# Optimization experiments

Hardware: AMD Instinct MI355X
Metric: run time of the kernel (lower is better)

The kernel has to match this reference:

```python
import jax, jax.numpy as jnp
import numpy as np

EPS = 1e-12


def _phi(e):
    # e: [C, L] -> pairwise euclidean distances [C, C], diagonal zeroed
    sq = jnp.sum(e * e, axis=1)                      # [C]
    prod = e @ e.T                                   # [C, C]
    d2 = sq[:, None] + sq[None, :] - 2.0 * prod
    d = jnp.sqrt(jnp.clip(d2, EPS, None))
    C = e.shape[0]
    return d * (1.0 - jnp.eye(C, dtype=e.dtype))


def setup_inputs() -> dict:
    key = jax.random.key(0)
    k1, k2, k3 = jax.random.split(key, 3)
    N, C, L = 64, 512, 256
    le_student = jax.random.normal(k1, (N, C, L), dtype=jnp.float32)
    le_teacher = jax.random.normal(k2, (N, C, L), dtype=jnp.float32)
    targets = jax.random.randint(k3, (N, C), 0, 2, dtype=jnp.int32)
    return {"le_student": le_student, "le_teacher": le_teacher, "targets": targets}


def reference(le_student, le_teacher, targets):
    N, C, L = le_student.shape
    m = targets.astype(le_student.dtype)             # [N, C] 0/1 mask
    es = le_student * m[:, :, None]                  # zero out negative rows
    et = le_teacher * m[:, :, None]

    Ds = jax.vmap(_phi)(es)                          # [N, C, C]
    Dt = jax.vmap(_phi)(et)                          # [N, C, C]

    eye = jnp.eye(C, dtype=m.dtype)
    pm = m[:, :, None] * m[:, None, :]               # pairs of positive rows
    offdiag = pm * (1.0 - eye)                       # off-diagonal positive pairs

    npos = jnp.sum(m, axis=1)                        # [N]
    cnt = npos * (npos - 1.0)                        # entries with d > 0 in submatrix
    valid = npos > 1.0
    safe_cnt = jnp.maximum(cnt, 1.0)

    mean_s = jnp.sum(Ds * offdiag, axis=(1, 2)) / safe_cnt
    mean_t = jax.lax.stop_gradient(jnp.sum(Dt * offdiag, axis=(1, 2)) / safe_cnt)
    mean_s = jnp.where(valid, mean_s, 1.0)
    mean_t = jnp.where(valid, mean_t, 1.0)

    d = Ds / mean_s[:, None, None]
    td = jax.lax.stop_gradient(Dt / mean_t[:, None, None])

    diff = d - td
    adiff = jnp.abs(diff)
    huber = jnp.where(adiff < 1.0, 0.5 * diff * diff, adiff - 0.5)

    per = jnp.sum(huber * pm, axis=(1, 2)) / jnp.maximum(npos, 1.0)
    return jnp.sum(jnp.where(valid, per, 0.0))
```

## Files before the change

### kernel.cpp

```cpp
#include <hip/hip_runtime.h>
#include <hip/hip_bf16.h>
#include <hip/hip_fp16.h>
#include <math.h>

#define NB 64
#define CC 512
#define LL 256

typedef __attribute__((ext_vector_type(4))) float floatx4;
typedef __attribute__((ext_vector_type(8))) short short8;

static __device__ __forceinline__ unsigned f2bf2(float x, float y) {
    __hip_bfloat162 h = __float22bfloat162_rn(make_float2(x, y));
    union { __hip_bfloat162 h; unsigned u; } c; c.h = h;
    return c.u;
}
static __device__ __forceinline__ unsigned f2h(float x) {
    __half h = __float2half_rn(x);
    union { __half h; unsigned short u; } c; c.h = h;
    return (unsigned)c.u;
}
static __device__ __forceinline__ float h2f(unsigned u) {
    union { unsigned short u; __half h; } c; c.u = (unsigned short)u;
    return __half2float(c.h);
}

__global__ __launch_bounds__(256) void prep_kernel(
    const int* __restrict__ targets,
    int* __restrict__ idx, int* __restrict__ npos,
    float* __restrict__ sumS, float* __restrict__ sumT, float* __restrict__ out)
{
    const int n = blockIdx.x, tid = threadIdx.x;
    __shared__ int s_cnt[8], s_off[8];
    const int w = tid >> 6, lane = tid & 63;
    const int* tg = targets + n * CC;
    const bool p0 = tg[tid] != 0;
    const bool p1 = tg[tid + 256] != 0;
    const unsigned long long m0 = __ballot(p0);
    const unsigned long long m1 = __ballot(p1);
    if (lane == 0) { s_cnt[w] = __popcll(m0); s_cnt[4 + w] = __popcll(m1); }
    __syncthreads();
    if (tid == 0) {
        int a = 0;
        for (int i = 0; i < 8; ++i) { s_off[i] = a; a += s_cnt[i]; }
        npos[n] = a;
        sumS[n] = 0.0f; sumT[n] = 0.0f;
        if (n == 0) out[0] = 0.0f;
    }
    __syncthreads();
    const unsigned long long below = (1ull << lane) - 1ull;
    if (p0) idx[n * CC + s_off[w] + __popcll(m0 & below)] = tid;
    if (p1) idx[n * CC + s_off[4 + w] + __popcll(m1 & below)] = tid + 256;
}

static __device__ __forceinline__ bool decode_tile(int t, int u, int& tI, int& tJ) {
    if (t >= (u * (u + 1)) >> 1) return false;
    tI = 0;
    while (t >= u - tI) { t -= u - tI; ++tI; }
    tJ = tI + t;
    return true;
}

__global__ __launch_bounds__(256) void dist_kernel(
    const float* __restrict__ S, const float* __restrict__ T,
    const int* __restrict__ idx, const int* __restrict__ npos,
    float* __restrict__ sumS, float* __restrict__ sumT,
    unsigned* __restrict__ D)
{
    const int bx = blockIdx.x;
    const int n = bx / 36;
    const int np = npos[n];
    if (np < 2) return;
    int tI, tJ;
    if (!decode_tile(bx - n * 36, (np + 63) >> 6, tI, tJ)) return;
    const bool diag = (tI == tJ);

    __shared__ __align__(16) unsigned short lds[4][2][64][40];
    __shared__ float s_norm[4][64];
    __shared__ float redA[4], redB[4];

    const int tid = threadIdx.x;
    const int w = tid >> 6, lane = tid & 63;

    const bool stager = (!diag) || ((w & 1) == 0);
    const char* Pbase = (const char*)(((w >> 1) ? T : S) + (size_t)n * CC * LL);
    const int tileBase = ((w & 1) ? tJ : tI) * 64;
    const int r8 = lane >> 3, c8 = lane & 7;
    unsigned off_[8];
    #pragma unroll
    for (int i = 0; i < 8; ++i) {
        const int gk = tileBase + r8 + 8 * i;
        const int row = idx[n * CC + ((gk < np) ? gk : 0)];
        off_[i] = (unsigned)(row * LL * 4 + c8 * 16);
    }

    float4 pre[8];
    float nprt[8];
    #pragma unroll
    for (int i = 0; i < 8; ++i) nprt[i] = 0.0f;
    if (stager) {
        #pragma unroll
        for (int i = 0; i < 8; ++i) pre[i] = *(const float4*)(Pbase + off_[i]);
    }

    const int m16 = lane & 15, quad = lane >> 4;
    const int bufB = diag ? 0 : 1;
    const int wrow = w * 16;

    floatx4 accS[4], accT[4];
    #pragma unroll
    for (int c = 0; c < 4; ++c) {
        accS[c][0] = 0; accS[c][1] = 0; accS[c][2] = 0; accS[c][3] = 0;
        accT[c][0] = 0; accT[c][1] = 0; accT[c][2] = 0; accT[c][3] = 0;
    }

    for (int kk = 0; kk < 8; ++kk) {
        const int pb = kk & 1;
        if (stager) {
            #pragma unroll
            for (int i = 0; i < 8; ++i) {
                nprt[i] += pre[i].x * pre[i].x + pre[i].y * pre[i].y +
                           pre[i].z * pre[i].z + pre[i].w * pre[i].w;
                *(uint2*)&lds[w][pb][r8 + 8 * i][c8 * 4] =
                    make_uint2(f2bf2(pre[i].x, pre[i].y), f2bf2(pre[i].z, pre[i].w));
            }
        }
        __syncthreads();
        if (stager && kk < 7) {
            #pragma unroll
            for (int i = 0; i < 8; ++i)
                pre[i] = *(const float4*)(Pbase + off_[i] + (kk + 1) * 128);
        }
        const int aoff = (wrow + m16) * 40 + quad * 8;
        const short8 a_s = *(const short8*)(&lds[0][pb][0][0] + aoff);
        const short8 a_t = *(const short8*)(&lds[2][pb][0][0] + aoff);
        #pragma unroll
        for (int c = 0; c < 4; ++c) {
            const int boff = (c * 16 + m16) * 40 + quad * 8;
            const short8 b_s = *(const short8*)(&lds[bufB][pb][0][0] + boff);
            const short8 b_t = *(const short8*)(&lds[2 + bufB][pb][0][0] + boff);
            accS[c] = __builtin_amdgcn_mfma_f32_16x16x32_bf16(a_s, b_s, accS[c], 0, 0, 0);
            accT[c] = __builtin_amdgcn_mfma_f32_16x16x32_bf16(a_t, b_t, accT[c], 0, 0, 0);
        }
    }

    if (stager) {
        #pragma unroll
        for (int i = 0; i < 8; ++i) {
            float v = nprt[i];
            v += __shfl_xor(v, 1); v += __shfl_xor(v, 2); v += __shfl_xor(v, 4);
            if (c8 == 0) s_norm[w][r8 + 8 * i] = v;
        }
    }
    __syncthreads();

    unsigned* Dn = D + ((size_t)bx << 12);
    float l0 = 0.0f, l1 = 0.0f;
    #pragma unroll
    for (int c = 0; c < 4; ++c) {
        const int colL = c * 16 + m16;
        const int gj = tJ * 64 + colL;
        const float nBs = s_norm[bufB][colL];
        const float nBt = s_norm[2 + bufB][colL];
        #pragma unroll
        for (int r = 0; r < 4; ++r) {
            const int rowL = wrow + quad * 4 + r;
            const int gi = tI * 64 + rowL;
            const float ds = sqrtf(fmaxf(s_norm[0][rowL] + nBs - 2.0f * accS[c][r], 1e-12f));
            const float dt = sqrtf(fmaxf(s_norm[2][rowL] + nBt - 2.0f * accT[c][r], 1e-12f));
            if (gi < np && gj < np && gi != gj) { l0 += ds; l1 += dt; }
            Dn[rowL * 64 + colL] = f2h(ds) | (f2h(dt) << 16);
        }
    }

    #pragma unroll
    for (int o = 32; o; o >>= 1) { l0 += __shfl_down(l0, o); l1 += __shfl_down(l1, o); }
    if (lane == 0) { redA[w] = l0; redB[w] = l1; }
    __syncthreads();
    if (tid == 0) {
        const float wgt = diag ? 1.0f : 2.0f;
        atomicAdd(&sumS[n], wgt * (redA[0] + redA[1] + redA[2] + redA[3]));
        atomicAdd(&sumT[n], wgt * (redB[0] + redB[1] + redB[2] + redB[3]));
    }
}

__global__ __launch_bounds__(256) void huber_kernel(
    const unsigned* __restrict__ D, const int* __restrict__ npos,
    const float* __restrict__ sumS, const float* __restrict__ sumT,
    float* __restrict__ out)
{
    const int bx = blockIdx.x;
    const int n = bx / 36;
    const int np = npos[n];
    if (np < 2) return;
    int tI, tJ;
    if (!decode_tile(bx - n * 36, (np + 63) >> 6, tI, tJ)) return;

    const float cnt = (float)np * (float)(np - 1);
    const float inv_ms = cnt / sumS[n];
    const float inv_mt = cnt / sumT[n];

    const uint4* Dn = (const uint4*)(D + ((size_t)bx << 12));
    const int tid = threadIdx.x;

    float h = 0.0f;
    #pragma unroll
    for (int it = 0; it < 4; ++it) {
        const int e4 = it * 256 + tid;
        const uint4 v = Dn[e4];
        const unsigned vv[4] = { v.x, v.y, v.z, v.w };
        const int e0 = e4 * 4;
        #pragma unroll
        for (int k = 0; k < 4; ++k) {
            const int e = e0 + k;
            const int gi = tI * 64 + (e >> 6);
            const int gj = tJ * 64 + (e & 63);
            if (gi < np && gj < np && gi != gj) {
                const float ds = h2f(vv[k] & 0xffffu);
                const float dt = h2f(vv[k] >> 16);
                const float diff = ds * inv_ms - dt * inv_mt;
                const float ad = fabsf(diff);
                h += (ad < 1.0f) ? 0.5f * diff * diff : ad - 0.5f;
            }
        }
    }

    #pragma unroll
    for (int o = 32; o; o >>= 1) h += __shfl_down(h, o);
    __shared__ float red[4];
    const int w = tid >> 6, lane = tid & 63;
    if (lane == 0) red[w] = h;
    __syncthreads();
    if (tid == 0) {
        const float wgt = (tI == tJ) ? 1.0f : 2.0f;
        atomicAdd(out, wgt * (red[0] + red[1] + red[2] + red[3]) / (float)np);
    }
}

extern "C" void kernel_launch(void* const* d_in, const int* in_sizes, int n_in,
                              void* d_out, int out_size, void* d_ws, size_t ws_size,
                              hipStream_t stream) {
    const float* S = (const float*)d_in[0];
    const float* T = (const float*)d_in[1];
    const int* targets = (const int*)d_in[2];
    float* out = (float*)d_out;

    char* p = (char*)d_ws;
    int* idx = (int*)p;        p += (size_t)NB * CC * 4;
    int* npos = (int*)p;       p += NB * 4;
    float* sumS = (float*)p;   p += NB * 4;
    float* sumT = (float*)p;   p += NB * 4;
    p = (char*)(((size_t)p + 255) & ~(size_t)255);
    unsigned* D = (unsigned*)p;

    prep_kernel<<<NB, 256, 0, stream>>>(targets, idx, npos, sumS, sumT, out);
    dist_kernel<<<NB * 36, 256, 0, stream>>>(S, T, idx, npos, sumS, sumT, D);
    huber_kernel<<<NB * 36, 256, 0, stream>>>(D, npos, sumS, sumT, out);
}
```

Measured before the change: 137.4 us.

## Split student and teacher distance tiles into separate blocks with interleaved tile order

Each dist block now computes only one matrix (student or teacher), which doubles the grid to 72*NB blocks. Per-block LDS, staging work and accumulator registers are halved. Block indexing now places the batch index in the low bits, so blocks that early-exit on the same tile index sit next to each other, and the fp16 distance outputs go to separate S and T buffers. The trade-off is twice as many blocks, each doing the idx gather, index decoding and an atomic, plus two separate reads in the huber pass.

```diff
diff --git a/kernel.cpp b/kernel.cpp
--- a/kernel.cpp
+++ b/kernel.cpp
@@ -15,10 +15,10 @@
     union { __hip_bfloat162 h; unsigned u; } c; c.h = h;
     return c.u;
 }
-static __device__ __forceinline__ unsigned f2h(float x) {
+static __device__ __forceinline__ unsigned short f2h(float x) {
     __half h = __float2half_rn(x);
     union { __half h; unsigned short u; } c; c.h = h;
-    return (unsigned)c.u;
+    return c.u;
 }
 static __device__ __forceinline__ float h2f(unsigned u) {
     union { unsigned short u; __half h; } c; c.u = (unsigned short)u;
@@ -65,159 +65,151 @@
     const float* __restrict__ S, const float* __restrict__ T,
     const int* __restrict__ idx, const int* __restrict__ npos,
     float* __restrict__ sumS, float* __restrict__ sumT,
-    unsigned* __restrict__ D)
+    unsigned short* __restrict__ Ds, unsigned short* __restrict__ Dt)
 {
     const int bx = blockIdx.x;
-    const int n = bx / 36;
+    const int n = bx & (NB - 1);
+    const int q = bx >> 6;
+    const int mat = q & 1, t = q >> 1;
     const int np = npos[n];
     if (np < 2) return;
     int tI, tJ;
-    if (!decode_tile(bx - n * 36, (np + 63) >> 6, tI, tJ)) return;
+    if (!decode_tile(t, (np + 63) >> 6, tI, tJ)) return;
     const bool diag = (tI == tJ);
 
-    __shared__ __align__(16) unsigned short lds[4][2][64][40];
-    __shared__ float s_norm[4][64];
-    __shared__ float redA[4], redB[4];
+    __shared__ __align__(16) unsigned short lds[2][2][64][40];
+    __shared__ float s_norm[2][64];
+    __shared__ float red[4];
 
     const int tid = threadIdx.x;
     const int w = tid >> 6, lane = tid & 63;
 
-    const bool stager = (!diag) || ((w & 1) == 0);
-    const char* Pbase = (const char*)(((w >> 1) ? T : S) + (size_t)n * CC * LL);
-    const int tileBase = ((w & 1) ? tJ : tI) * 64;
-    const int r8 = lane >> 3, c8 = lane & 7;
-    unsigned off_[8];
-    #pragma unroll
-    for (int i = 0; i < 8; ++i) {
-        const int gk = tileBase + r8 + 8 * i;
-        const int row = idx[n * CC + ((gk < np) ? gk : 0)];
-        off_[i] = (unsigned)(row * LL * 4 + c8 * 16);
-    }
-
-    float4 pre[8];
-    float nprt[8];
-    #pragma unroll
-    for (int i = 0; i < 8; ++i) nprt[i] = 0.0f;
+    const float* P = (mat ? T : S) + (size_t)n * CC * LL;
+    unsigned short* Dout = (mat ? Dt : Ds) + (((size_t)t * NB + n) << 12);
+    float* sumP = mat ? sumT : sumS;
+
+    const int srow = w * 32 + (lane >> 1);
+    const int half = lane & 1;
+    const bool stager = diag ? (srow < 64) : true;
+    const int ab = srow >> 6, rloc = srow & 63;
+    const int gk = (ab ? tJ : tI) * 64 + rloc;
+    const int row = idx[n * CC + ((gk < np) ? gk : 0)];
+    const char* rp = (const char*)P + (size_t)row * (LL * 4) + half * 64;
+
+    float4 pre[4];
+    float nsum = 0.0f;
     if (stager) {
         #pragma unroll
-        for (int i = 0; i < 8; ++i) pre[i] = *(const float4*)(Pbase + off_[i]);
+        for (int i = 0; i < 4; ++i) pre[i] = *(const float4*)(rp + i * 16);
     }
 
     const int m16 = lane & 15, quad = lane >> 4;
     const int bufB = diag ? 0 : 1;
     const int wrow = w * 16;
 
-    floatx4 accS[4], accT[4];
-    #pragma unroll
-    for (int c = 0; c < 4; ++c) {
-        accS[c][0] = 0; accS[c][1] = 0; accS[c][2] = 0; accS[c][3] = 0;
-        accT[c][0] = 0; accT[c][1] = 0; accT[c][2] = 0; accT[c][3] = 0;
-    }
+    floatx4 acc[4];
+    #pragma unroll
+    for (int c = 0; c < 4; ++c) { acc[c][0] = 0; acc[c][1] = 0; acc[c][2] = 0; acc[c][3] = 0; }
 
     for (int kk = 0; kk < 8; ++kk) {
         const int pb = kk & 1;
         if (stager) {
             #pragma unroll
-            for (int i = 0; i < 8; ++i) {
-                nprt[i] += pre[i].x * pre[i].x + pre[i].y * pre[i].y +
-                           pre[i].z * pre[i].z + pre[i].w * pre[i].w;
-                *(uint2*)&lds[w][pb][r8 + 8 * i][c8 * 4] =
-                    make_uint2(f2bf2(pre[i].x, pre[i].y), f2bf2(pre[i].z, pre[i].w));
-            }
+            for (int i = 0; i < 4; ++i)
+                nsum += pre[i].x * pre[i].x + pre[i].y * pre[i].y +
+                        pre[i].z * pre[i].z + pre[i].w * pre[i].w;
+            unsigned short* dst = &lds[ab][pb][rloc][half * 16];
+            *(uint2*)(dst + 0)  = make_uint2(f2bf2(pre[0].x, pre[0].y), f2bf2(pre[0].z, pre[0].w));
+            *(uint2*)(dst + 4)  = make_uint2(f2bf2(pre[1].x, pre[1].y), f2bf2(pre[1].z, pre[1].w));
+            *(uint2*)(dst + 8)  = make_uint2(f2bf2(pre[2].x, pre[2].y), f2bf2(pre[2].z, pre[2].w));
+            *(uint2*)(dst + 12) = make_uint2(f2bf2(pre[3].x, pre[3].y), f2bf2(pre[3].z, pre[3].w));
         }
         __syncthreads();
         if (stager && kk < 7) {
             #pragma unroll
-            for (int i = 0; i < 8; ++i)
-                pre[i] = *(const float4*)(Pbase + off_[i] + (kk + 1) * 128);
-        }
-        const int aoff = (wrow + m16) * 40 + quad * 8;
-        const short8 a_s = *(const short8*)(&lds[0][pb][0][0] + aoff);
-        const short8 a_t = *(const short8*)(&lds[2][pb][0][0] + aoff);
+            for (int i = 0; i < 4; ++i)
+                pre[i] = *(const float4*)(rp + (kk + 1) * 128 + i * 16);
+        }
+        const short8 a = *(const short8*)&lds[0][pb][wrow + m16][quad * 8];
         #pragma unroll
         for (int c = 0; c < 4; ++c) {
-            const int boff = (c * 16 + m16) * 40 + quad * 8;
-            const short8 b_s = *(const short8*)(&lds[bufB][pb][0][0] + boff);
-            const short8 b_t = *(const short8*)(&lds[2 + bufB][pb][0][0] + boff);
-            accS[c] = __builtin_amdgcn_mfma_f32_16x16x32_bf16(a_s, b_s, accS[c], 0, 0, 0);
-            accT[c] = __builtin_amdgcn_mfma_f32_16x16x32_bf16(a_t, b_t, accT[c], 0, 0, 0);
+            const short8 b = *(const short8*)&lds[bufB][pb][c * 16 + m16][quad * 8];
+            acc[c] = __builtin_amdgcn_mfma_f32_16x16x32_bf16(a, b, acc[c], 0, 0, 0);
         }
     }
 
     if (stager) {
-        #pragma unroll
-        for (int i = 0; i < 8; ++i) {
-            float v = nprt[i];
-            v += __shfl_xor(v, 1); v += __shfl_xor(v, 2); v += __shfl_xor(v, 4);
-            if (c8 == 0) s_norm[w][r8 + 8 * i] = v;
-        }
-    }
-    __syncthreads();
-
-    unsigned* Dn = D + ((size_t)bx << 12);
-    float l0 = 0.0f, l1 = 0.0f;
+        const float v = nsum + __shfl_xor(nsum, 1);
+        if (half == 0) s_norm[ab][rloc] = v;
+    }
+    __syncthreads();
+
+    float l0 = 0.0f;
     #pragma unroll
     for (int c = 0; c < 4; ++c) {
         const int colL = c * 16 + m16;
         const int gj = tJ * 64 + colL;
-        const float nBs = s_norm[bufB][colL];
-        const float nBt = s_norm[2 + bufB][colL];
+        const float nB = s_norm[bufB][colL];
         #pragma unroll
         for (int r = 0; r < 4; ++r) {
             const int rowL = wrow + quad * 4 + r;
             const int gi = tI * 64 + rowL;
-            const float ds = sqrtf(fmaxf(s_norm[0][rowL] + nBs - 2.0f * accS[c][r], 1e-12f));
-            const float dt = sqrtf(fmaxf(s_norm[2][rowL] + nBt - 2.0f * accT[c][r], 1e-12f));
-            if (gi < np && gj < np && gi != gj) { l0 += ds; l1 += dt; }
-            Dn[rowL * 64 + colL] = f2h(ds) | (f2h(dt) << 16);
-        }
-    }
-
-    #pragma unroll
-    for (int o = 32; o; o >>= 1) { l0 += __shfl_down(l0, o); l1 += __shfl_down(l1, o); }
-    if (lane == 0) { redA[w] = l0; redB[w] = l1; }
+            const float d = sqrtf(fmaxf(s_norm[0][rowL] + nB - 2.0f * acc[c][r], 1e-12f));
+            if (gi < np && gj < np && gi != gj) l0 += d;
+            Dout[rowL * 64 + colL] = f2h(d);
+        }
+    }
+
+    #pragma unroll
+    for (int o = 32; o; o >>= 1) l0 += __shfl_down(l0, o);
+    if (lane == 0) red[w] = l0;
     __syncthreads();
     if (tid == 0) {
         const float wgt = diag ? 1.0f : 2.0f;
-        atomicAdd(&sumS[n], wgt * (redA[0] + redA[1] + redA[2] + redA[3]));
-        atomicAdd(&sumT[n], wgt * (redB[0] + redB[1] + redB[2] + redB[3]));
+        atomicAdd(sumP + n, wgt * (red[0] + red[1] + red[2] + red[3]));
     }
 }
 
 __global__ __launch_bounds__(256) void huber_kernel(
-    const unsigned* __restrict__ D, const int* __restrict__ npos,
+    const unsigned short* __restrict__ Ds, const unsigned short* __restrict__ Dt,
+    const int* __restrict__ npos,
     const float* __restrict__ sumS, const float* __restrict__ sumT,
     float* __restrict__ out)
 {
     const int bx = blockIdx.x;
-    const int n = bx / 36;
+    const int n = bx & (NB - 1), t = bx >> 6;
     const int np = npos[n];
     if (np < 2) return;
     int tI, tJ;
-    if (!decode_tile(bx - n * 36, (np + 63) >> 6, tI, tJ)) return;
+    if (!decode_tile(t, (np + 63) >> 6, tI, tJ)) return;
 
     const float cnt = (float)np * (float)(np - 1);
     const float inv_ms = cnt / sumS[n];
     const float inv_mt = cnt / sumT[n];
 
-    const uint4* Dn = (const uint4*)(D + ((size_t)bx << 12));
+    const size_t slot = ((size_t)t * NB + n) << 12;
+    const uint4* ps = (const uint4*)(Ds + slot);
+    const uint4* pt = (const uint4*)(Dt + slot);
     const int tid = threadIdx.x;
 
     float h = 0.0f;
     #pragma unroll
-    for (int it = 0; it < 4; ++it) {
-        const int e4 = it * 256 + tid;
-        const uint4 v = Dn[e4];
-        const unsigned vv[4] = { v.x, v.y, v.z, v.w };
-        const int e0 = e4 * 4;
-        #pragma unroll
-        for (int k = 0; k < 4; ++k) {
+    for (int it = 0; it < 2; ++it) {
+        const int g = it * 256 + tid;
+        const uint4 a = ps[g];
+        const uint4 b = pt[g];
+        const unsigned aw[4] = { a.x, a.y, a.z, a.w };
+        const unsigned bw[4] = { b.x, b.y, b.z, b.w };
+        const int e0 = g * 8;
+        #pragma unroll
+        for (int k = 0; k < 8; ++k) {
             const int e = e0 + k;
             const int gi = tI * 64 + (e >> 6);
             const int gj = tJ * 64 + (e & 63);
             if (gi < np && gj < np && gi != gj) {
-                const float ds = h2f(vv[k] & 0xffffu);
-                const float dt = h2f(vv[k] >> 16);
+                const unsigned wa = aw[k >> 1], wb = bw[k >> 1];
+                const float ds = h2f((k & 1) ? (wa >> 16) : (wa & 0xffffu));
+                const float dt = h2f((k & 1) ? (wb >> 16) : (wb & 0xffffu));
                 const float diff = ds * inv_ms - dt * inv_mt;
                 const float ad = fabsf(diff);
                 h += (ad < 1.0f) ? 0.5f * diff * diff : ad - 0.5f;
@@ -251,9 +243,10 @@
     float* sumS = (float*)p;   p += NB * 4;
     float* sumT = (float*)p;   p += NB * 4;
     p = (char*)(((size_t)p + 255) & ~(size_t)255);
-    unsigned* D = (unsigned*)p;
+    unsigned short* Ds = (unsigned short*)p;   p += (size_t)36 * NB * 4096 * 2;
+    unsigned short* Dt = (unsigned short*)p;
 
     prep_kernel<<<NB, 256, 0, stream>>>(targets, idx, npos, sumS, sumT, out);
-    dist_kernel<<<NB * 36, 256, 0, stream>>>(S, T, idx, npos, sumS, sumT, D);
-    huber_kernel<<<NB * 36, 256, 0, stream>>>(D, npos, sumS, sumT, out);
-}
+    dist_kernel<<<72 * NB, 256, 0, stream>>>(S, T, idx, npos, sumS, sumT, Ds, Dt);
+    huber_kernel<<<36 * NB, 256, 0, stream>>>(Ds, Dt, npos, sumS, sumT, out);
+}
```

Result: faster. 124.8 us (-9.2%).
